# Optimization experiments

Measured on AMD Instinct MI355X. Metric: run time of the kernel, lower is better.

## Reference

```python
import jax, jax.numpy as jnp
import numpy as np

DIM = 1536
N_HEADS = 12
HEAD_DIM = 128
EPS = 1e-6
MAX_ATTN = 32760      # local_attn_size(21) * 1560
CACHE_SIZE = 32760
CUR_START = 4680      # 3 frames * 1560 already in cache
TWO_PI = 6.283185307179586


def rms_norm(x, g, eps=EPS):
    x32 = x.astype(jnp.float32)
    y = x32 * jax.lax.rsqrt(jnp.mean(x32 * x32, axis=-1, keepdims=True) + eps)
    return y.astype(x.dtype) * g


def causal_rope(x, grid_sizes, freqs, start_frame):
    # x: [B, s, n, d]; freqs: angles [1024, d//2] (torch stores exp(i*theta); we store theta)
    B, s, n, d = x.shape
    c = d // 2
    c3 = c // 3
    f_ang = freqs[:, : c - 2 * c3]
    h_ang = freqs[:, c - 2 * c3 : c - c3]
    w_ang = freqs[:, c - c3 :]
    outs = []
    grid_np = np.asarray(grid_sizes)
    for i in range(B):
        F, H, W = (int(v) for v in grid_np[i])
        seq = F * H * W
        ang = jnp.concatenate([
            jnp.broadcast_to(f_ang[start_frame : start_frame + F][:, None, None, :], (F, H, W, c - 2 * c3)),
            jnp.broadcast_to(h_ang[:H][None, :, None, :], (F, H, W, c3)),
            jnp.broadcast_to(w_ang[:W][None, None, :, :], (F, H, W, c3)),
        ], axis=-1).reshape(seq, 1, c)
        cos, sin = jnp.cos(ang), jnp.sin(ang)
        xi = x[i, :seq].astype(jnp.float32).reshape(seq, n, c, 2)
        a, b = xi[..., 0], xi[..., 1]
        rot = jnp.stack([a * cos - b * sin, a * sin + b * cos], axis=-1).reshape(seq, n, d)
        outs.append(jnp.concatenate([rot, x[i, seq:].astype(jnp.float32)], axis=0))
    return jnp.stack(outs).astype(x.dtype)


def setup_inputs() -> dict:
    key = jax.random.key(0)
    ks = jax.random.split(key, 16)
    B, S = 1, 1560
    w = lambda k: jax.random.normal(k, (DIM, DIM), jnp.float32) * 0.02
    return {
        "x": jax.random.normal(ks[0], (B, S, DIM), jnp.float32),
        "freqs": jax.random.uniform(ks[1], (1024, HEAD_DIM // 2), jnp.float32) * TWO_PI,
        "wq": w(ks[2]), "bq": jnp.zeros((DIM,), jnp.float32),
        "wk": w(ks[3]), "bk": jnp.zeros((DIM,), jnp.float32),
        "wv": w(ks[4]), "bv": jnp.zeros((DIM,), jnp.float32),
        "wo": w(ks[5]), "bo": jnp.zeros((DIM,), jnp.float32),
        "gq": jnp.ones((DIM,), jnp.float32),
        "gk": jnp.ones((DIM,), jnp.float32),
        "kv_cache_k": jax.random.normal(ks[6], (B, CACHE_SIZE, N_HEADS, HEAD_DIM), jnp.float32),
        "kv_cache_v": jax.random.normal(ks[7], (B, CACHE_SIZE, N_HEADS, HEAD_DIM), jnp.float32),
        "grid_sizes": jnp.array([[1, 30, 52]], jnp.int64 if jax.config.jax_enable_x64 else jnp.int32),
        "seq_lens": jnp.array([1560], jnp.int32),
        "current_start": CUR_START,
    }


def reference(x, freqs, wq, bq, wk, bk, wv, bv, wo, bo, gq, gk,
              kv_cache_k, kv_cache_v, grid_sizes, seq_lens, current_start):
    b, s = x.shape[:2]
    n, d = N_HEADS, HEAD_DIM
    q = rms_norm(x @ wq.T + bq, gq).reshape(b, s, n, d)
    k = rms_norm(x @ wk.T + bk, gk).reshape(b, s, n, d)
    v = (x @ wv.T + bv).reshape(b, s, n, d)

    grid_np = np.asarray(grid_sizes)
    frame_seqlen = int(grid_np[0, 1]) * int(grid_np[0, 2])  # 1560
    start_frame = int(current_start) // frame_seqlen
    rq = causal_rope(q, grid_sizes, freqs, start_frame)
    rk = causal_rope(k, grid_sizes, freqs, start_frame)

    # cache in sync (global_end==local_end==current_start), no-eviction branch
    cur_start = int(current_start)
    cur_end = cur_start + s
    k_cache = kv_cache_k.at[:, cur_start:cur_end].set(rk)
    v_cache = kv_cache_v.at[:, cur_start:cur_end].set(v)

    win_start = max(0, cur_end - MAX_ATTN)
    kw = k_cache[:, win_start:cur_end]  # [B, W, n, d]
    vw = v_cache[:, win_start:cur_end]

    scale = 1.0 / np.sqrt(d).astype(np.float32)
    scores = jnp.einsum("bqnd,bknd->bnqk", rq, kw) * scale
    attn = jax.nn.softmax(scores, axis=-1)
    out = jnp.einsum("bnqk,bknd->bqnd", attn, vw).reshape(b, s, n * d)
    return out @ wo.T + bo
```

## Files before the change

### kernel.cpp

```cpp
#include <hip/hip_runtime.h>
#include <math.h>

typedef unsigned short ushort_t;
typedef __attribute__((ext_vector_type(8))) short bf16x8;
typedef __attribute__((ext_vector_type(4))) float f32x4;

#define DIM    1536
#define NH     12
#define HD     128
#define SEQ    1560
#define CURS   4680
#define NKEY   6240
#define GW     52
#define SFRAME 3
#define EPSV   1e-6f
#define QSCALE 0.08838834764831845f
#define KSPLIT 2
#define NCHUNK 98
#define CPS    49
#define QPAD   1600

__device__ __forceinline__ ushort_t f2bf(float f) {
    union { float f; unsigned int u; } x; x.f = f;
    unsigned int r = x.u + 0x7fffu + ((x.u >> 16) & 1u);
    return (ushort_t)(r >> 16);
}

template<int OUTBF>
__global__ __launch_bounds__(256) void gemm_bf16(
    const float* __restrict__ A, const float* __restrict__ W,
    const float* __restrict__ bias, void* __restrict__ Cout,
    int M, int N, int K)
{
    __shared__ ushort_t As[64][40];
    __shared__ ushort_t Bs[64][40];
    const int t = threadIdx.x;
    const int w = t >> 6, l = t & 63, quad = l >> 4, l15 = l & 15;
    const int bm = blockIdx.y * 64, bn = blockIdx.x * 64;
    const int wm = (w & 1) * 32, wn = (w >> 1) * 32;
    const int lrow = t >> 2, lk = (t & 3) * 8;

    const float* Ap = A + (size_t)min(bm + lrow, M - 1) * K + lk;
    const float* Wp = W + (size_t)(bn + lrow) * K + lk;

    f32x4 acc[4] = {};

    for (int k0 = 0; k0 < K; k0 += 32) {
        float4 a0 = *(const float4*)(Ap + k0);
        float4 a1 = *(const float4*)(Ap + k0 + 4);
        float4 b0 = *(const float4*)(Wp + k0);
        float4 b1 = *(const float4*)(Wp + k0 + 4);
        __syncthreads();
        union { ushort_t u[8]; bf16x8 v; } ua, ub;
        ua.u[0]=f2bf(a0.x); ua.u[1]=f2bf(a0.y); ua.u[2]=f2bf(a0.z); ua.u[3]=f2bf(a0.w);
        ua.u[4]=f2bf(a1.x); ua.u[5]=f2bf(a1.y); ua.u[6]=f2bf(a1.z); ua.u[7]=f2bf(a1.w);
        ub.u[0]=f2bf(b0.x); ub.u[1]=f2bf(b0.y); ub.u[2]=f2bf(b0.z); ub.u[3]=f2bf(b0.w);
        ub.u[4]=f2bf(b1.x); ub.u[5]=f2bf(b1.y); ub.u[6]=f2bf(b1.z); ub.u[7]=f2bf(b1.w);
        *(bf16x8*)&As[lrow][lk] = ua.v;
        *(bf16x8*)&Bs[lrow][lk] = ub.v;
        __syncthreads();
        bf16x8 af0 = *(const bf16x8*)&As[wm +      l15][quad*8];
        bf16x8 af1 = *(const bf16x8*)&As[wm + 16 + l15][quad*8];
        bf16x8 bf0 = *(const bf16x8*)&Bs[wn +      l15][quad*8];
        bf16x8 bf1 = *(const bf16x8*)&Bs[wn + 16 + l15][quad*8];
        acc[0] = __builtin_amdgcn_mfma_f32_16x16x32_bf16(af0, bf0, acc[0], 0,0,0);
        acc[1] = __builtin_amdgcn_mfma_f32_16x16x32_bf16(af0, bf1, acc[1], 0,0,0);
        acc[2] = __builtin_amdgcn_mfma_f32_16x16x32_bf16(af1, bf0, acc[2], 0,0,0);
        acc[3] = __builtin_amdgcn_mfma_f32_16x16x32_bf16(af1, bf1, acc[3], 0,0,0);
    }
    #pragma unroll
    for (int mi = 0; mi < 2; ++mi)
    #pragma unroll
    for (int ni = 0; ni < 2; ++ni) {
        const int col = bn + wn + ni*16 + l15;
        const float bcol = bias[col];
        f32x4 a = acc[mi*2+ni];
        #pragma unroll
        for (int r = 0; r < 4; ++r) {
            const int row = bm + wm + mi*16 + quad*4 + r;
            if (row < M) {
                float v = a[r] + bcol;
                if (OUTBF) ((ushort_t*)Cout)[(size_t)row * N + col] = f2bf(v);
                else       ((float*)   Cout)[(size_t)row * N + col] = v;
            }
        }
    }
}

__global__ __launch_bounds__(256)
void rmsnorm_rope(const float* __restrict__ buf, const float* __restrict__ g,
                  const float* __restrict__ freqs, ushort_t* __restrict__ out,
                  float scale)
{
    const int tok = blockIdx.x;
    const int t = threadIdx.x;
    const float* row = buf + (size_t)tok * DIM;

    float2 xv[3];
    float ss = 0.f;
    #pragma unroll
    for (int i = 0; i < 3; ++i) {
        xv[i] = ((const float2*)row)[t + 256*i];
        ss += xv[i].x*xv[i].x + xv[i].y*xv[i].y;
    }
    #pragma unroll
    for (int off = 32; off > 0; off >>= 1) ss += __shfl_xor(ss, off);
    __shared__ float part[4];
    __shared__ float invs;
    if ((t & 63) == 0) part[t >> 6] = ss;
    __syncthreads();
    if (t == 0) invs = rsqrtf((part[0]+part[1]+part[2]+part[3]) * (1.0f/DIM) + EPSV);
    __syncthreads();
    const float inv = invs * scale;
    const int hh = tok / GW;
    const int ww = tok % GW;
    #pragma unroll
    for (int i = 0; i < 3; ++i) {
        const int p = t + 256*i;
        const int j = p & 63;
        const int rsel = (j < 22) ? SFRAME : ((j < 43) ? hh : ww);
        const float ang = freqs[rsel*64 + j];
        float sn, cs;
        sincosf(ang, &sn, &cs);
        const float a = xv[i].x * inv * g[2*p];
        const float b = xv[i].y * inv * g[2*p+1];
        const unsigned int lo = f2bf(a*cs - b*sn);
        const unsigned int hi = f2bf(a*sn + b*cs);
        ((unsigned int*)out)[(size_t)tok*768 + p] = (hi << 16) | lo;
    }
}

__global__ __launch_bounds__(256)
void kwin_k(const float* __restrict__ kc, const ushort_t* __restrict__ kb,
            ushort_t* __restrict__ Kw)
{
    const int tid = blockIdx.x * 256 + threadIdx.x;
    const int dc = tid & 15;
    const int hp = tid >> 4;
    const int p = hp % NKEY;
    const int h = hp / NKEY;
    ushort_t* outp = Kw + (size_t)tid * 8;
    if (p >= CURS) {
        *(bf16x8*)outp = *(const bf16x8*)(kb + (size_t)(p - CURS)*DIM + h*HD + dc*8);
    } else {
        const float* src = kc + ((size_t)p * NH + h) * HD + dc*8;
        float4 f0 = *(const float4*)src, f1 = *(const float4*)(src + 4);
        union { ushort_t u[8]; bf16x8 v; } uu;
        uu.u[0]=f2bf(f0.x); uu.u[1]=f2bf(f0.y); uu.u[2]=f2bf(f0.z); uu.u[3]=f2bf(f0.w);
        uu.u[4]=f2bf(f1.x); uu.u[5]=f2bf(f1.y); uu.u[6]=f2bf(f1.z); uu.u[7]=f2bf(f1.w);
        *(bf16x8*)outp = uu.v;
    }
}

__global__ __launch_bounds__(256)
void kwin_v(const float* __restrict__ vc, const ushort_t* __restrict__ vb,
            ushort_t* __restrict__ Vwt)
{
    __shared__ ushort_t tile[64][40];
    const int t = threadIdx.x;
    const int bp = blockIdx.x, bd = blockIdx.y, h = blockIdx.z;
    const int p_loc = t >> 2, ds0 = (t & 3) * 8;
    const int pr = min(bp*64 + p_loc, NKEY-1);
    const int d = bd*32 + ds0;
    union { ushort_t u[8]; bf16x8 v; } uu;
    if (pr >= CURS) {
        uu.v = *(const bf16x8*)(vb + (size_t)(pr - CURS)*DIM + h*HD + d);
    } else {
        const float* src = vc + ((size_t)pr*NH + h)*HD + d;
        float4 f0 = *(const float4*)src, f1 = *(const float4*)(src+4);
        uu.u[0]=f2bf(f0.x); uu.u[1]=f2bf(f0.y); uu.u[2]=f2bf(f0.z); uu.u[3]=f2bf(f0.w);
        uu.u[4]=f2bf(f1.x); uu.u[5]=f2bf(f1.y); uu.u[6]=f2bf(f1.z); uu.u[7]=f2bf(f1.w);
    }
    *(bf16x8*)&tile[p_loc][ds0] = uu.v;
    __syncthreads();
    const int d_loc = t >> 3, ps = (t & 7) * 8;
    if (bp*64 + ps < NKEY) {
        union { ushort_t u[8]; bf16x8 v; } oo;
        #pragma unroll
        for (int i = 0; i < 8; ++i) oo.u[i] = tile[ps + i][d_loc];
        *(bf16x8*)(Vwt + ((size_t)h*HD + bd*32 + d_loc) * NKEY + bp*64 + ps) = oo.v;
    }
}

__global__ __launch_bounds__(256)
void attn_kernel(const ushort_t* __restrict__ qb, const ushort_t* __restrict__ Kw,
                 const ushort_t* __restrict__ Vwt, float* __restrict__ Op,
                 float* __restrict__ Ms, float* __restrict__ Ls)
{
    __shared__ ushort_t Ks[64][136];
    __shared__ ushort_t Vs[128][72];
    __shared__ float    Sc[64][68];
    __shared__ ushort_t Pb[64][72];
    __shared__ float mst[64], lst[64], alf[64];

    const int t = threadIdx.x;
    const int w = t >> 6, l = t & 63, quad = l >> 4, l15 = l & 15;
    const int h = blockIdx.y;
    const int q0 = blockIdx.x * 64;
    const int z = blockIdx.z;

    bf16x8 qf[4];
    {
        const int qrow = min(q0 + w*16 + l15, SEQ-1);
        const ushort_t* qp = qb + ((size_t)qrow*NH + h)*HD;
        #pragma unroll
        for (int s = 0; s < 4; ++s) qf[s] = *(const bf16x8*)(qp + s*32 + quad*8);
    }
    f32x4 o[8] = {};
    if (t < 64) { mst[t] = -1e30f; lst[t] = 0.f; }

    const ushort_t* Kwh = Kw  + (size_t)h * NKEY * HD;
    const ushort_t* Vwh = Vwt + (size_t)h * HD * NKEY;
    const int key_st = t >> 2, kd0 = (t & 3) * 32;
    const int vd = t >> 1,     vk0 = (t & 1) * 32;

    for (int c = z*CPS; c < (z+1)*CPS; ++c) {
        const int p0 = c * 64;
        bf16x8 kr[4], vr[4];
        {
            const ushort_t* kp = Kwh + (size_t)min(p0 + key_st, NKEY-1) * HD + kd0;
            #pragma unroll
            for (int i = 0; i < 4; ++i) kr[i] = *(const bf16x8*)(kp + i*8);
            const ushort_t* vp = Vwh + (size_t)vd * NKEY;
            #pragma unroll
            for (int i = 0; i < 4; ++i) {
                const int pk = min(p0 + vk0 + i*8, NKEY-8);
                vr[i] = *(const bf16x8*)(vp + pk);
            }
        }
        __syncthreads();
        #pragma unroll
        for (int i = 0; i < 4; ++i) *(bf16x8*)&Ks[key_st][kd0 + i*8] = kr[i];
        #pragma unroll
        for (int i = 0; i < 4; ++i) *(bf16x8*)&Vs[vd][vk0 + i*8] = vr[i];
        __syncthreads();

        f32x4 sf[4];
        #pragma unroll
        for (int kb = 0; kb < 4; ++kb) { f32x4 zz = {0.f,0.f,0.f,0.f}; sf[kb] = zz; }
        #pragma unroll
        for (int s = 0; s < 4; ++s) {
            #pragma unroll
            for (int kb = 0; kb < 4; ++kb) {
                bf16x8 kf = *(const bf16x8*)&Ks[kb*16 + l15][s*32 + quad*8];
                sf[kb] = __builtin_amdgcn_mfma_f32_16x16x32_bf16(qf[s], kf, sf[kb], 0,0,0);
            }
        }
        #pragma unroll
        for (int kb = 0; kb < 4; ++kb) {
            const int pkey = p0 + kb*16 + l15;
            const bool valid = pkey < NKEY;
            #pragma unroll
            for (int r = 0; r < 4; ++r)
                Sc[w*16 + quad*4 + r][kb*16 + l15] = valid ? sf[kb][r] : -1e30f;
        }
        __syncthreads();

        {
            const int row = t >> 2, seg = t & 3;
            float sv[16];
            #pragma unroll
            for (int i = 0; i < 4; ++i) {
                float4 s4 = *(const float4*)&Sc[row][seg*16 + i*4];
                sv[i*4+0]=s4.x; sv[i*4+1]=s4.y; sv[i*4+2]=s4.z; sv[i*4+3]=s4.w;
            }
            float mx = sv[0];
            #pragma unroll
            for (int i = 1; i < 16; ++i) mx = fmaxf(mx, sv[i]);
            mx = fmaxf(mx, __shfl_xor(mx, 1));
            mx = fmaxf(mx, __shfl_xor(mx, 2));
            const float mo = mst[row];
            const float mn = fmaxf(mo, mx);
            float sum = 0.f;
            union { ushort_t u[8]; bf16x8 v; } pa, pc;
            #pragma unroll
            for (int i = 0; i < 8; ++i) { float e = __expf(sv[i]   - mn); sum += e; pa.u[i] = f2bf(e); }
            #pragma unroll
            for (int i = 0; i < 8; ++i) { float e = __expf(sv[8+i] - mn); sum += e; pc.u[i] = f2bf(e); }
            sum += __shfl_xor(sum, 1);
            sum += __shfl_xor(sum, 2);
            *(bf16x8*)&Pb[row][seg*16]     = pa.v;
            *(bf16x8*)&Pb[row][seg*16 + 8] = pc.v;
            if (seg == 0) {
                const float al = __expf(mo - mn);
                lst[row] = lst[row]*al + sum;
                mst[row] = mn;
                alf[row] = al;
            }
        }
        __syncthreads();

        {
            float ar[4];
            #pragma unroll
            for (int r = 0; r < 4; ++r) ar[r] = alf[w*16 + quad*4 + r];
            #pragma unroll
            for (int nb = 0; nb < 8; ++nb)
                #pragma unroll
                for (int r = 0; r < 4; ++r) o[nb][r] *= ar[r];
            #pragma unroll
            for (int ks = 0; ks < 2; ++ks) {
                bf16x8 pf = *(const bf16x8*)&Pb[w*16 + l15][ks*32 + quad*8];
                #pragma unroll
                for (int nb = 0; nb < 8; ++nb) {
                    bf16x8 vf = *(const bf16x8*)&Vs[nb*16 + l15][ks*32 + quad*8];
                    o[nb] = __builtin_amdgcn_mfma_f32_16x16x32_bf16(pf, vf, o[nb], 0,0,0);
                }
            }
        }
    }
    __syncthreads();
    {
        float* Opz = Op + (size_t)z * QPAD * NH * HD;
        #pragma unroll
        for (int nb = 0; nb < 8; ++nb) {
            const int col = nb*16 + l15;
            #pragma unroll
            for (int r = 0; r < 4; ++r) {
                const int row = q0 + w*16 + quad*4 + r;
                Opz[((size_t)row*NH + h)*HD + col] = o[nb][r];
            }
        }
        if (t < 64) {
            const int row = q0 + t;
            Ms[(size_t)z*QPAD*NH + row*NH + h] = mst[t];
            Ls[(size_t)z*QPAD*NH + row*NH + h] = lst[t];
        }
    }
}

__global__ __launch_bounds__(256)
void merge_kernel(const float* __restrict__ Op, const float* __restrict__ Ms,
                  const float* __restrict__ Ls, float* __restrict__ abuf)
{
    const int tid = blockIdx.x*256 + threadIdx.x;
    const int dq = tid & 31;
    const int h = (tid >> 5) % NH;
    const int q = tid / (NH*32);
    const size_t sidx = (size_t)q*NH + h;
    const float m0 = Ms[sidx], m1 = Ms[(size_t)QPAD*NH + sidx];
    const float l0 = Ls[sidx], l1 = Ls[(size_t)QPAD*NH + sidx];
    const float mm = fmaxf(m0, m1);
    const float w0 = __expf(m0 - mm), w1 = __expf(m1 - mm);
    const float inv = 1.0f / (l0*w0 + l1*w1);
    const size_t oidx = sidx*HD + dq*4;
    float4 a = *(const float4*)(Op + oidx);
    float4 b = *(const float4*)(Op + (size_t)QPAD*NH*HD + oidx);
    float4 r;
    r.x = (a.x*w0 + b.x*w1)*inv;
    r.y = (a.y*w0 + b.y*w1)*inv;
    r.z = (a.z*w0 + b.z*w1)*inv;
    r.w = (a.w*w0 + b.w*w1)*inv;
    *(float4*)(abuf + (size_t)q*DIM + h*HD + dq*4) = r;
}

extern "C" void kernel_launch(void* const* d_in, const int* in_sizes, int n_in,
                              void* d_out, int out_size, void* d_ws, size_t ws_size,
                              hipStream_t stream)
{
    const float* x     = (const float*)d_in[0];
    const float* freqs = (const float*)d_in[1];
    const float* wq    = (const float*)d_in[2];
    const float* bq    = (const float*)d_in[3];
    const float* wk    = (const float*)d_in[4];
    const float* bk    = (const float*)d_in[5];
    const float* wv    = (const float*)d_in[6];
    const float* bv    = (const float*)d_in[7];
    const float* wo    = (const float*)d_in[8];
    const float* bo    = (const float*)d_in[9];
    const float* gq    = (const float*)d_in[10];
    const float* gk    = (const float*)d_in[11];
    const float* kck   = (const float*)d_in[12];
    const float* kcv   = (const float*)d_in[13];

    char* ws = (char*)d_ws;
    const size_t SZ_B16 = (size_t)SEQ*DIM*2;
    const size_t SZ_KW  = (size_t)NH*NKEY*HD*2;
    const size_t SZ_OP  = (size_t)KSPLIT*QPAD*NH*HD*4;
    const size_t SZ_ST  = (size_t)KSPLIT*QPAD*NH*4;
    const size_t SZ_F32 = (size_t)SEQ*DIM*4;

    ushort_t* qb  = (ushort_t*)(ws);
    ushort_t* kb  = (ushort_t*)(ws + SZ_B16);
    ushort_t* vb  = (ushort_t*)(ws + 2*SZ_B16);
    ushort_t* Kw  = (ushort_t*)(ws + 3*SZ_B16);
    ushort_t* Vwt = (ushort_t*)(ws + 3*SZ_B16 + SZ_KW);
    float*    Opb = (float*)   (ws + 3*SZ_B16 + 2*SZ_KW);
    float*    Msp = (float*)   (ws + 3*SZ_B16 + 2*SZ_KW + SZ_OP);
    float*    Lsp = (float*)   (ws + 3*SZ_B16 + 2*SZ_KW + SZ_OP + SZ_ST);
    float*    abuf= (float*)   (ws + 3*SZ_B16 + 2*SZ_KW + SZ_OP + 2*SZ_ST);
    float*    qf  = Opb;
    float*    kf  = (float*)((char*)Opb + SZ_F32);

    dim3 blk(256);
    dim3 gg(DIM/64, (SEQ+63)/64);

    hipLaunchKernelGGL((gemm_bf16<0>), gg, blk, 0, stream, x, wq, bq, (void*)qf, SEQ, DIM, DIM);
    hipLaunchKernelGGL((gemm_bf16<0>), gg, blk, 0, stream, x, wk, bk, (void*)kf, SEQ, DIM, DIM);
    hipLaunchKernelGGL((gemm_bf16<1>), gg, blk, 0, stream, x, wv, bv, (void*)vb, SEQ, DIM, DIM);
    hipLaunchKernelGGL(rmsnorm_rope, dim3(SEQ), blk, 0, stream, qf, gq, freqs, qb, QSCALE);
    hipLaunchKernelGGL(rmsnorm_rope, dim3(SEQ), blk, 0, stream, kf, gk, freqs, kb, 1.0f);
    hipLaunchKernelGGL(kwin_k, dim3(NH*NKEY*16/256), blk, 0, stream, kck, kb, Kw);
    hipLaunchKernelGGL(kwin_v, dim3(98, 4, NH), blk, 0, stream, kcv, vb, Vwt);
    hipLaunchKernelGGL(attn_kernel, dim3((SEQ+63)/64, NH, KSPLIT), blk, 0, stream,
                       qb, Kw, Vwt, Opb, Msp, Lsp);
    hipLaunchKernelGGL(merge_kernel, dim3(SEQ*NH*32/256), blk, 0, stream, Opb, Msp, Lsp, abuf);
    hipLaunchKernelGGL((gemm_bf16<0>), gg, blk, 0, stream, abuf, wo, bo, d_out, SEQ, DIM, DIM);
}
```

Baseline: 839.4 us.

## Pre-convert operands to bf16 and use fused 128x128 QKV GEMM with direct LDS loads

```diff
diff --git a/kernel.cpp b/kernel.cpp
--- a/kernel.cpp
+++ b/kernel.cpp
@@ -19,6 +19,7 @@
 #define NCHUNK 98
 #define CPS    49
 #define QPAD   1600
+#define MPAD   1664
 
 __device__ __forceinline__ ushort_t f2bf(float f) {
     union { float f; unsigned int u; } x; x.f = f;
@@ -26,62 +27,92 @@
     return (ushort_t)(r >> 16);
 }
 
-template<int OUTBF>
-__global__ __launch_bounds__(256) void gemm_bf16(
-    const float* __restrict__ A, const float* __restrict__ W,
-    const float* __restrict__ bias, void* __restrict__ Cout,
-    int M, int N, int K)
-{
-    __shared__ ushort_t As[64][40];
-    __shared__ ushort_t Bs[64][40];
+__device__ __forceinline__ void gld_lds16(const ushort_t* gsrc, ushort_t* ldst) {
+    __builtin_amdgcn_global_load_lds(
+        (const __attribute__((address_space(1))) unsigned int*)gsrc,
+        (__attribute__((address_space(3))) unsigned int*)ldst,
+        16, 0, 0);
+}
+
+__global__ __launch_bounds__(256)
+void f32_to_bf16_k(const float* __restrict__ in, ushort_t* __restrict__ out, int n8)
+{
+    const int i = blockIdx.x * 256 + threadIdx.x;
+    if (i >= n8) return;
+    float4 a = ((const float4*)in)[2*i];
+    float4 b = ((const float4*)in)[2*i + 1];
+    union { ushort_t u[8]; bf16x8 v; } uu;
+    uu.u[0]=f2bf(a.x); uu.u[1]=f2bf(a.y); uu.u[2]=f2bf(a.z); uu.u[3]=f2bf(a.w);
+    uu.u[4]=f2bf(b.x); uu.u[5]=f2bf(b.y); uu.u[6]=f2bf(b.z); uu.u[7]=f2bf(b.w);
+    ((bf16x8*)out)[i] = uu.v;
+}
+
+template<int QKV>
+__global__ __launch_bounds__(256) void gemm128(
+    const ushort_t* __restrict__ A, const ushort_t* __restrict__ B,
+    const float* __restrict__ b0, const float* __restrict__ b1, const float* __restrict__ b2,
+    float* __restrict__ outQ, float* __restrict__ outK, ushort_t* __restrict__ outV,
+    int M, int K)
+{
+    __shared__ ushort_t As[128*32];
+    __shared__ ushort_t Bs[128*32];
+
     const int t = threadIdx.x;
     const int w = t >> 6, l = t & 63, quad = l >> 4, l15 = l & 15;
-    const int bm = blockIdx.y * 64, bn = blockIdx.x * 64;
-    const int wm = (w & 1) * 32, wn = (w >> 1) * 32;
-    const int lrow = t >> 2, lk = (t & 3) * 8;
-
-    const float* Ap = A + (size_t)min(bm + lrow, M - 1) * K + lk;
-    const float* Wp = W + (size_t)(bn + lrow) * K + lk;
-
-    f32x4 acc[4] = {};
+    const int bm = blockIdx.y * 128;
+    const int bn = blockIdx.x * 128;
+    const int wm = (w & 1) << 6, wn = (w >> 1) << 6;
+
+    const int srow = (w << 5) + (l >> 2);
+    const int scol = (l & 3) << 3;
+    const ushort_t* Ag = A + (size_t)(bm + srow) * K + scol;
+    const ushort_t* Bg = B + (size_t)(bn + srow) * K + scol;
+    ushort_t* AsB = &As[w << 10];
+    ushort_t* BsB = &Bs[w << 10];
+
+    f32x4 acc[4][4] = {};
 
     for (int k0 = 0; k0 < K; k0 += 32) {
-        float4 a0 = *(const float4*)(Ap + k0);
-        float4 a1 = *(const float4*)(Ap + k0 + 4);
-        float4 b0 = *(const float4*)(Wp + k0);
-        float4 b1 = *(const float4*)(Wp + k0 + 4);
-        __syncthreads();
-        union { ushort_t u[8]; bf16x8 v; } ua, ub;
-        ua.u[0]=f2bf(a0.x); ua.u[1]=f2bf(a0.y); ua.u[2]=f2bf(a0.z); ua.u[3]=f2bf(a0.w);
-        ua.u[4]=f2bf(a1.x); ua.u[5]=f2bf(a1.y); ua.u[6]=f2bf(a1.z); ua.u[7]=f2bf(a1.w);
-        ub.u[0]=f2bf(b0.x); ub.u[1]=f2bf(b0.y); ub.u[2]=f2bf(b0.z); ub.u[3]=f2bf(b0.w);
-        ub.u[4]=f2bf(b1.x); ub.u[5]=f2bf(b1.y); ub.u[6]=f2bf(b1.z); ub.u[7]=f2bf(b1.w);
-        *(bf16x8*)&As[lrow][lk] = ua.v;
-        *(bf16x8*)&Bs[lrow][lk] = ub.v;
-        __syncthreads();
-        bf16x8 af0 = *(const bf16x8*)&As[wm +      l15][quad*8];
-        bf16x8 af1 = *(const bf16x8*)&As[wm + 16 + l15][quad*8];
-        bf16x8 bf0 = *(const bf16x8*)&Bs[wn +      l15][quad*8];
-        bf16x8 bf1 = *(const bf16x8*)&Bs[wn + 16 + l15][quad*8];
-        acc[0] = __builtin_amdgcn_mfma_f32_16x16x32_bf16(af0, bf0, acc[0], 0,0,0);
-        acc[1] = __builtin_amdgcn_mfma_f32_16x16x32_bf16(af0, bf1, acc[1], 0,0,0);
-        acc[2] = __builtin_amdgcn_mfma_f32_16x16x32_bf16(af1, bf0, acc[2], 0,0,0);
-        acc[3] = __builtin_amdgcn_mfma_f32_16x16x32_bf16(af1, bf1, acc[3], 0,0,0);
-    }
+        __syncthreads();
+        gld_lds16(Ag + k0,          AsB);
+        gld_lds16(Ag + k0 + 16*K,   AsB + 512);
+        gld_lds16(Bg + k0,          BsB);
+        gld_lds16(Bg + k0 + 16*K,   BsB + 512);
+        __syncthreads();
+
+        bf16x8 af[4], bfv[4];
+        #pragma unroll
+        for (int i = 0; i < 4; ++i) {
+            af[i]  = *(const bf16x8*)&As[(wm + i*16 + l15) * 32 + quad*8];
+            bfv[i] = *(const bf16x8*)&Bs[(wn + i*16 + l15) * 32 + quad*8];
+        }
+        #pragma unroll
+        for (int mi = 0; mi < 4; ++mi)
+            #pragma unroll
+            for (int ni = 0; ni < 4; ++ni)
+                acc[mi][ni] = __builtin_amdgcn_mfma_f32_16x16x32_bf16(af[mi], bfv[ni], acc[mi][ni], 0,0,0);
+    }
+
+    int mat, c0;
+    if (QKV) { mat = blockIdx.x / 12; c0 = (blockIdx.x % 12) * 128; }
+    else     { mat = 0;               c0 = blockIdx.x * 128; }
+    const float* bias = QKV ? (mat == 0 ? b0 : (mat == 1 ? b1 : b2)) : b0;
+    float* outF = (QKV && mat == 1) ? outK : outQ;
+
     #pragma unroll
-    for (int mi = 0; mi < 2; ++mi)
-    #pragma unroll
-    for (int ni = 0; ni < 2; ++ni) {
-        const int col = bn + wn + ni*16 + l15;
-        const float bcol = bias[col];
-        f32x4 a = acc[mi*2+ni];
-        #pragma unroll
-        for (int r = 0; r < 4; ++r) {
-            const int row = bm + wm + mi*16 + quad*4 + r;
-            if (row < M) {
-                float v = a[r] + bcol;
-                if (OUTBF) ((ushort_t*)Cout)[(size_t)row * N + col] = f2bf(v);
-                else       ((float*)   Cout)[(size_t)row * N + col] = v;
+    for (int ni = 0; ni < 4; ++ni) {
+        const int col = c0 + wn + ni*16 + l15;
+        const float bc = bias[col];
+        #pragma unroll
+        for (int mi = 0; mi < 4; ++mi) {
+            #pragma unroll
+            for (int r = 0; r < 4; ++r) {
+                const int row = bm + wm + mi*16 + quad*4 + r;
+                if (row < M) {
+                    const float v = acc[mi][ni][r] + bc;
+                    if (QKV && mat == 2) outV[(size_t)row * DIM + col] = f2bf(v);
+                    else                 outF[(size_t)row * DIM + col] = v;
+                }
             }
         }
     }
@@ -331,7 +362,7 @@
 
 __global__ __launch_bounds__(256)
 void merge_kernel(const float* __restrict__ Op, const float* __restrict__ Ms,
-                  const float* __restrict__ Ls, float* __restrict__ abuf)
+                  const float* __restrict__ Ls, ushort_t* __restrict__ abufb)
 {
     const int tid = blockIdx.x*256 + threadIdx.x;
     const int dq = tid & 31;
@@ -346,12 +377,12 @@
     const size_t oidx = sidx*HD + dq*4;
     float4 a = *(const float4*)(Op + oidx);
     float4 b = *(const float4*)(Op + (size_t)QPAD*NH*HD + oidx);
-    float4 r;
-    r.x = (a.x*w0 + b.x*w1)*inv;
-    r.y = (a.y*w0 + b.y*w1)*inv;
-    r.z = (a.z*w0 + b.z*w1)*inv;
-    r.w = (a.w*w0 + b.w*w1)*inv;
-    *(float4*)(abuf + (size_t)q*DIM + h*HD + dq*4) = r;
+    ushort4 r;
+    r.x = f2bf((a.x*w0 + b.x*w1)*inv);
+    r.y = f2bf((a.y*w0 + b.y*w1)*inv);
+    r.z = f2bf((a.z*w0 + b.z*w1)*inv);
+    r.w = f2bf((a.w*w0 + b.w*w1)*inv);
+    *(ushort4*)(abufb + (size_t)q*DIM + h*HD + dq*4) = r;
 }
 
 extern "C" void kernel_launch(void* const* d_in, const int* in_sizes, int n_in,
@@ -378,7 +409,7 @@
     const size_t SZ_KW  = (size_t)NH*NKEY*HD*2;
     const size_t SZ_OP  = (size_t)KSPLIT*QPAD*NH*HD*4;
     const size_t SZ_ST  = (size_t)KSPLIT*QPAD*NH*4;
-    const size_t SZ_F32 = (size_t)SEQ*DIM*4;
+    const size_t SZ_AB  = (size_t)MPAD*DIM*2;
 
     ushort_t* qb  = (ushort_t*)(ws);
     ushort_t* kb  = (ushort_t*)(ws + SZ_B16);
@@ -388,22 +419,35 @@
     float*    Opb = (float*)   (ws + 3*SZ_B16 + 2*SZ_KW);
     float*    Msp = (float*)   (ws + 3*SZ_B16 + 2*SZ_KW + SZ_OP);
     float*    Lsp = (float*)   (ws + 3*SZ_B16 + 2*SZ_KW + SZ_OP + SZ_ST);
-    float*    abuf= (float*)   (ws + 3*SZ_B16 + 2*SZ_KW + SZ_OP + 2*SZ_ST);
-    float*    qf  = Opb;
-    float*    kf  = (float*)((char*)Opb + SZ_F32);
+    ushort_t* abufb=(ushort_t*)(ws + 3*SZ_B16 + 2*SZ_KW + SZ_OP + 2*SZ_ST);
+    ushort_t* wob = (ushort_t*)(ws + 3*SZ_B16 + 2*SZ_KW + SZ_OP + 2*SZ_ST + SZ_AB);
+    ushort_t* xb   = abufb;
+    ushort_t* Wqkv = Kw;
+    float*    qf   = Opb;
+    float*    kf   = Opb + (size_t)SEQ*DIM;
 
     dim3 blk(256);
-    dim3 gg(DIM/64, (SEQ+63)/64);
-
-    hipLaunchKernelGGL((gemm_bf16<0>), gg, blk, 0, stream, x, wq, bq, (void*)qf, SEQ, DIM, DIM);
-    hipLaunchKernelGGL((gemm_bf16<0>), gg, blk, 0, stream, x, wk, bk, (void*)kf, SEQ, DIM, DIM);
-    hipLaunchKernelGGL((gemm_bf16<1>), gg, blk, 0, stream, x, wv, bv, (void*)vb, SEQ, DIM, DIM);
+    const int XN8 = SEQ*DIM/8;
+    const int WN8 = DIM*DIM/8;
+    const size_t WE = (size_t)DIM*DIM;
+
+    hipLaunchKernelGGL(f32_to_bf16_k, dim3((XN8+255)/256), blk, 0, stream, x,  xb,           XN8);
+    hipLaunchKernelGGL(f32_to_bf16_k, dim3((WN8+255)/256), blk, 0, stream, wq, Wqkv,         WN8);
+    hipLaunchKernelGGL(f32_to_bf16_k, dim3((WN8+255)/256), blk, 0, stream, wk, Wqkv + WE,    WN8);
+    hipLaunchKernelGGL(f32_to_bf16_k, dim3((WN8+255)/256), blk, 0, stream, wv, Wqkv + 2*WE,  WN8);
+    hipLaunchKernelGGL(f32_to_bf16_k, dim3((WN8+255)/256), blk, 0, stream, wo, wob,          WN8);
+
+    hipLaunchKernelGGL((gemm128<1>), dim3(36, 13), blk, 0, stream,
+                       xb, Wqkv, bq, bk, bv, qf, kf, vb, SEQ, DIM);
+
     hipLaunchKernelGGL(rmsnorm_rope, dim3(SEQ), blk, 0, stream, qf, gq, freqs, qb, QSCALE);
     hipLaunchKernelGGL(rmsnorm_rope, dim3(SEQ), blk, 0, stream, kf, gk, freqs, kb, 1.0f);
     hipLaunchKernelGGL(kwin_k, dim3(NH*NKEY*16/256), blk, 0, stream, kck, kb, Kw);
     hipLaunchKernelGGL(kwin_v, dim3(98, 4, NH), blk, 0, stream, kcv, vb, Vwt);
     hipLaunchKernelGGL(attn_kernel, dim3((SEQ+63)/64, NH, KSPLIT), blk, 0, stream,
                        qb, Kw, Vwt, Opb, Msp, Lsp);
-    hipLaunchKernelGGL(merge_kernel, dim3(SEQ*NH*32/256), blk, 0, stream, Opb, Msp, Lsp, abuf);
-    hipLaunchKernelGGL((gemm_bf16<0>), gg, blk, 0, stream, abuf, wo, bo, d_out, SEQ, DIM, DIM);
-}
+    hipLaunchKernelGGL(merge_kernel, dim3(SEQ*NH*32/256), blk, 0, stream, Opb, Msp, Lsp, abufb);
+
+    hipLaunchKernelGGL((gemm128<0>), dim3(12, 13), blk, 0, stream,
+                       abufb, wob, bo, bo, bo, (float*)d_out, (float*)d_out, (ushort_t*)nullptr, SEQ, DIM);
+}
```

Result: faster. 726.8 us (-13.4%).
